# Kernel tuning notes

Hardware: AMD Instinct MI355X
Metric: run time of the kernel (lower is better)

The kernel has to match this reference:

```python
import jax, jax.numpy as jnp
import numpy as np

DIM, H, C = 1024, 16, 64  # dim, num_heads, head_width
B, N = 2, 2048
EPS = 1e-5


def setup_inputs() -> dict:
    key = jax.random.key(0)
    ks = jax.random.split(key, 8)
    x = jax.random.normal(ks[0], (B, N, DIM), dtype=jnp.float32)
    bias = jax.random.normal(ks[1], (B, H, N, N), dtype=jnp.float32)
    mask = jax.random.randint(ks[2], (B, N), 0, 2, dtype=jnp.int32)
    s = DIM ** -0.5
    return {
        'x': x,
        'bias': bias,
        'mask': mask,
        'ln_w': jnp.ones((DIM,), jnp.float32),
        'ln_b': jnp.zeros((DIM,), jnp.float32),
        'w_qkv': jax.random.normal(ks[3], (3 * DIM, DIM), jnp.float32) * s,
        'w_o': jax.random.normal(ks[4], (DIM, DIM), jnp.float32) * s,
        'b_o': jnp.zeros((DIM,), jnp.float32),
        'w_g': jax.random.normal(ks[5], (DIM, DIM), jnp.float32) * s,
        'b_g': jnp.ones((DIM,), jnp.float32),
    }


def reference(x, bias, mask, ln_w, ln_b, w_qkv, w_o, b_o, w_g, b_g):
    # LayerNorm (eps=1e-5)
    mu = jnp.mean(x, axis=-1, keepdims=True)
    var = jnp.mean(jnp.square(x - mu), axis=-1, keepdims=True)
    xn = (x - mu) * jax.lax.rsqrt(var + EPS) * ln_w + ln_b

    # QKV projection (no bias): (B,N,3*DIM) -> (B,H,N,3C), chunk last dim
    t = jnp.einsum('bnd,ed->bne', xn, w_qkv)
    t = t.reshape(B, N, H, 3 * C).transpose(0, 2, 1, 3)  # (B,H,N,3C)
    q, k, v = t[..., :C], t[..., C:2 * C], t[..., 2 * C:]
    q = q * (C ** -0.5)

    # Biased, masked attention scores
    a = jnp.einsum('bhqc,bhkc->bhqk', q, k) + bias
    a = jnp.where(mask[:, None, None, :] == 0, -jnp.inf, a)
    a = jax.nn.softmax(a, axis=-1)

    y = jnp.einsum('bhqk,bhkc->bqhc', a, v).reshape(B, N, DIM)

    # Sigmoid gate from normalized x, then output projection
    g = jax.nn.sigmoid(jnp.einsum('bnd,ed->bne', xn, w_g) + b_g)
    y = g * y
    return jnp.einsum('bnd,ed->bne', y, w_o) + b_o
```

## Files before the change

### kernel.cpp

```cpp
#include <hip/hip_runtime.h>

#define DIMD 1024
#define NHEAD 16
#define CHD 64
#define BBATCH 2
#define NSEQ 2048
#define NTOK 4096
#define KDIM 1024
#define LOG2E 1.4426950408889634f

typedef __attribute__((ext_vector_type(4))) float f32x4;
typedef __attribute__((ext_vector_type(8))) short bf16x8;

__device__ __forceinline__ unsigned short f2bf(float f){
  unsigned int u = __float_as_uint(f);
  u += 0x7fffu + ((u >> 16) & 1u);
  return (unsigned short)(u >> 16);
}
__device__ __forceinline__ float bf2f(unsigned short u){
  return __uint_as_float(((unsigned int)u) << 16);
}

__device__ __forceinline__ void gl2lds16(const void* g, void* l){
  __builtin_amdgcn_global_load_lds(
      (const __attribute__((address_space(1))) unsigned int*)g,
      (__attribute__((address_space(3))) unsigned int*)l, 16, 0, 0);
}

template<int CTRL>
__device__ __forceinline__ float dppmv(float x){
  return __int_as_float(__builtin_amdgcn_mov_dpp(__float_as_int(x), CTRL, 0xF, 0xF, true));
}
__device__ __forceinline__ float rmax16(float x){
  x = fmaxf(x, dppmv<0xB1>(x));
  x = fmaxf(x, dppmv<0x4E>(x));
  x = fmaxf(x, dppmv<0x141>(x));
  x = fmaxf(x, dppmv<0x140>(x));
  return x;
}
__device__ __forceinline__ float rsum16(float x){
  x += dppmv<0xB1>(x);
  x += dppmv<0x4E>(x);
  x += dppmv<0x141>(x);
  x += dppmv<0x140>(x);
  return x;
}

__global__ __launch_bounds__(256) void pre_kernel(const float* __restrict__ x,
    const float* __restrict__ lw, const float* __restrict__ lb,
    const float* __restrict__ wqkv, const float* __restrict__ wg,
    const float* __restrict__ wo, unsigned short* __restrict__ xn,
    unsigned short* __restrict__ Wpack, unsigned short* __restrict__ Wo){
  __shared__ float red[8];
  int t = threadIdx.x;
  if (blockIdx.x < 4096){
    int row = blockIdx.x;
    const float4* xr = (const float4*)(x + (size_t)row * DIMD);
    float4 v = xr[t];
    float s  = v.x + v.y + v.z + v.w;
    float s2 = v.x*v.x + v.y*v.y + v.z*v.z + v.w*v.w;
#pragma unroll
    for (int m = 1; m < 64; m <<= 1){
      s  += __shfl_xor(s,  m, 64);
      s2 += __shfl_xor(s2, m, 64);
    }
    int wv = t >> 6;
    if ((t & 63) == 0){ red[wv] = s; red[wv + 4] = s2; }
    __syncthreads();
    s  = red[0] + red[1] + red[2] + red[3];
    s2 = red[4] + red[5] + red[6] + red[7];
    float mu  = s  * (1.0f / DIMD);
    float var = s2 * (1.0f / DIMD) - mu * mu;
    float rs  = rsqrtf(var + 1e-5f);
    float4 w  = ((const float4*)lw)[t];
    float4 bb = ((const float4*)lb)[t];
    ushort4 o;
    o.x = f2bf((v.x - mu) * rs * w.x + bb.x);
    o.y = f2bf((v.y - mu) * rs * w.y + bb.y);
    o.z = f2bf((v.z - mu) * rs * w.z + bb.z);
    o.w = f2bf((v.w - mu) * rs * w.w + bb.w);
    ((ushort4*)xn)[(size_t)row * 256 + t] = o;
  } else {
    int i = (blockIdx.x - 4096) * 256 + t;
    const int NQP   = 4096 * 1024 / 4;
    const int NQQKV = 3072 * 1024 / 4;
    float4 v; unsigned short* dst;
    if (i < NQP){
      const float* src = (i < NQQKV) ? (wqkv + (size_t)i * 4)
                                     : (wg + (size_t)(i - NQQKV) * 4);
      v = *(const float4*)src;
      dst = Wpack + (size_t)i * 4;
    } else {
      int j = i - NQP;
      v = ((const float4*)wo)[j];
      dst = Wo + (size_t)j * 4;
    }
    ushort4 o = { f2bf(v.x), f2bf(v.y), f2bf(v.z), f2bf(v.w) };
    *(ushort4*)dst = o;
  }
}

__device__ __forceinline__ void gemm_stage(const unsigned short* __restrict__ A,
    const unsigned short* __restrict__ Bm, int m0, int n0, int kb, char* lds, int tid){
#pragma unroll
  for (int i = 0; i < 4; i++){
    int c  = i * 256 + tid;
    int cc = c & 511;
    int r  = cc >> 2, k4 = cc & 3;
    const unsigned short* src =
        ((c >> 9) ? (Bm + (size_t)(n0 + r) * KDIM) : (A + (size_t)(m0 + r) * KDIM))
        + kb + k4 * 8;
    gl2lds16(src, lds + c * 16);
  }
}

__device__ __forceinline__ void gemm_main(const unsigned short* __restrict__ A,
    const unsigned short* __restrict__ Bm, int m0, int n0, char* lds,
    f32x4 acc[4][4], int wm, int wn, int l16, int quad){
  int tid = threadIdx.x;
  gemm_stage(A, Bm, m0, n0, 0, lds, tid);
  for (int kt = 0; kt < 32; kt++){
    __syncthreads();
    if (kt + 1 < 32)
      gemm_stage(A, Bm, m0, n0, (kt + 1) * 32, lds + ((kt + 1) & 1) * 16384, tid);
    const char* Ab = lds + (kt & 1) * 16384;
    const char* Bb = Ab + 8192;
    bf16x8 af[4], bfr[4];
#pragma unroll
    for (int t2 = 0; t2 < 4; t2++){
      af[t2]  = *(const bf16x8*)(Ab + (wm + t2 * 16 + l16) * 64 + quad * 16);
      bfr[t2] = *(const bf16x8*)(Bb + (wn + t2 * 16 + l16) * 64 + quad * 16);
    }
#pragma unroll
    for (int mt = 0; mt < 4; mt++)
#pragma unroll
      for (int nt = 0; nt < 4; nt++)
        acc[mt][nt] = __builtin_amdgcn_mfma_f32_16x16x32_bf16(af[mt], bfr[nt], acc[mt][nt], 0, 0, 0);
  }
}

__global__ __launch_bounds__(256) void gemm_qkvg(const unsigned short* __restrict__ xn,
    const unsigned short* __restrict__ Wpack, const float* __restrict__ bg,
    unsigned short* __restrict__ Q, unsigned short* __restrict__ Ko,
    unsigned short* __restrict__ Vt, unsigned short* __restrict__ g){
  __shared__ char lds[32768];
  int tid = threadIdx.x, lane = tid & 63, wave = tid >> 6;
  int l16 = lane & 15, quad = lane >> 4;
  int wm = (wave & 1) * 64, wn = (wave >> 1) * 64;
  int m0 = blockIdx.y * 128, n0 = blockIdx.x * 128;
  f32x4 acc[4][4];
#pragma unroll
  for (int i = 0; i < 4; i++)
#pragma unroll
    for (int j = 0; j < 4; j++) acc[i][j] = (f32x4){0.f, 0.f, 0.f, 0.f};
  gemm_main(xn, Wpack, m0, n0, lds, acc, wm, wn, l16, quad);
  const float QSCALE = 0.125f * LOG2E;
#pragma unroll
  for (int mt = 0; mt < 4; mt++){
#pragma unroll
    for (int nt = 0; nt < 4; nt++){
      int col = n0 + wn + nt * 16 + l16;
#pragma unroll
      for (int reg = 0; reg < 4; reg++){
        int row = m0 + wm + mt * 16 + quad * 4 + reg;
        float val = acc[mt][nt][reg];
        int b = row >> 11, n = row & 2047;
        if (col < 3072){
          int h = col / 192;
          int r = col - h * 192;
          int bh = b * 16 + h;
          if (r < 64)
            Q[((size_t)bh * 2048 + n) * 64 + r] = f2bf(val * QSCALE);
          else if (r < 128)
            Ko[((size_t)bh * 2048 + n) * 64 + (r - 64)] = f2bf(val);
          else
            Vt[((size_t)bh * 64 + (r - 128)) * 2048 + n] = f2bf(val);
        } else {
          int d = col - 3072;
          float gv = 1.0f / (1.0f + __expf(-(val + bg[d])));
          g[(size_t)row * 1024 + d] = f2bf(gv);
        }
      }
    }
  }
}

__device__ __forceinline__ void attn_stage(const unsigned short* __restrict__ Kbh,
    const unsigned short* __restrict__ Vtbh, int kb, char* Kdst, char* Vdst, int tid){
#pragma unroll
  for (int i = 0; i < 2; i++){
    int l = i * 256 + tid;
    int n = l >> 3, cc = (l & 7) ^ (n & 7);
    gl2lds16(Kbh + (size_t)(kb + n) * 64 + cc * 8, Kdst + l * 16);
  }
#pragma unroll
  for (int i = 0; i < 2; i++){
    int l = i * 256 + tid;
    int c = l >> 3, cc = (l & 7) ^ (c & 7);
    gl2lds16(Vtbh + (size_t)c * 2048 + kb + cc * 8, Vdst + l * 16);
  }
}

__global__ __launch_bounds__(256) void attn_kernel(
    const unsigned short* __restrict__ Q, const unsigned short* __restrict__ Ko,
    const unsigned short* __restrict__ Vt, const float* __restrict__ bias,
    const int* __restrict__ mask, const unsigned short* __restrict__ g,
    unsigned short* __restrict__ yg){
  __shared__ char smem[40960];
  int tid = threadIdx.x, lane = tid & 63, wave = tid >> 6;
  int l16 = lane & 15, quad = lane >> 4;
  int qt = blockIdx.x, bh = blockIdx.y;
  int b = bh >> 4, h = bh & 15;

  const unsigned short* Qbh  = Q  + (size_t)bh * 2048 * 64;
  const unsigned short* Kbh  = Ko + (size_t)bh * 2048 * 64;
  const unsigned short* Vtbh = Vt + (size_t)bh * 64 * 2048;
  const float* biasw = bias + (size_t)bh * 2048 * 2048 + (size_t)(qt * 64 + wave * 16) * 2048;
  const int* maskb = mask + b * 2048;
  char* Pw = smem + 32768 + wave * 2048;

  bf16x8 qf[2];
  {
    const unsigned short* qrow = Qbh + (size_t)(qt * 64 + wave * 16 + l16) * 64;
    qf[0] = *(const bf16x8*)(qrow + quad * 8);
    qf[1] = *(const bf16x8*)(qrow + 32 + quad * 8);
  }

  f32x4 yacc[4];
#pragma unroll
  for (int ct = 0; ct < 4; ct++) yacc[ct] = (f32x4){0.f, 0.f, 0.f, 0.f};
  float m_run[4] = {-1e30f, -1e30f, -1e30f, -1e30f};
  float l_run[4] = {0.f, 0.f, 0.f, 0.f};

  float ba[4][4], bb[4][4];
  int mka[4], mkb[4];
  attn_stage(Kbh, Vtbh, 0, smem, smem + 16384, tid);
#pragma unroll
  for (int nt = 0; nt < 4; nt++){
    mka[nt] = maskb[nt * 16 + l16];
#pragma unroll
    for (int reg = 0; reg < 4; reg++)
      ba[nt][reg] = biasw[(size_t)(quad * 4 + reg) * 2048 + nt * 16 + l16];
  }

  auto body = [&](int kt, float (&cur)[4][4], int (&mcur)[4],
                  float (&nxt)[4][4], int (&mnxt)[4]){
    __syncthreads();
    int kb = kt * 64;
    if (kt + 1 < 32){
      attn_stage(Kbh, Vtbh, kb + 64, smem + (((kt + 1) & 1) << 13),
                 smem + 16384 + (((kt + 1) & 1) << 13), tid);
#pragma unroll
      for (int nt = 0; nt < 4; nt++){
        mnxt[nt] = maskb[kb + 64 + nt * 16 + l16];
#pragma unroll
        for (int reg = 0; reg < 4; reg++)
          nxt[nt][reg] = biasw[(size_t)(quad * 4 + reg) * 2048 + kb + 64 + nt * 16 + l16];
      }
    }
    const char* Kb_ = smem + ((kt & 1) << 13);
    const char* Vb_ = smem + 16384 + ((kt & 1) << 13);

    f32x4 s[4];
#pragma unroll
    for (int nt = 0; nt < 4; nt++) s[nt] = (f32x4){0.f, 0.f, 0.f, 0.f};
#pragma unroll
    for (int kk = 0; kk < 2; kk++)
#pragma unroll
      for (int nt = 0; nt < 4; nt++){
        int n = nt * 16 + l16;
        bf16x8 kf = *(const bf16x8*)(Kb_ + n * 128 + ((((kk << 2) + quad) ^ (n & 7)) << 4));
        s[nt] = __builtin_amdgcn_mfma_f32_16x16x32_bf16(qf[kk], kf, s[nt], 0, 0, 0);
      }
#pragma unroll
    for (int nt = 0; nt < 4; nt++){
      bool ok = (mcur[nt] != 0);
#pragma unroll
      for (int reg = 0; reg < 4; reg++){
        float v = fmaf(cur[nt][reg], LOG2E, s[nt][reg]);
        s[nt][reg] = ok ? v : -1e30f;
      }
    }
    float alpha[4], psum[4];
#pragma unroll
    for (int reg = 0; reg < 4; reg++){
      float m4 = fmaxf(fmaxf(s[0][reg], s[1][reg]), fmaxf(s[2][reg], s[3][reg]));
      m4 = rmax16(m4);
      float mn = fmaxf(m_run[reg], m4);
      alpha[reg] = __builtin_amdgcn_exp2f(m_run[reg] - mn);
      m_run[reg] = mn;
      psum[reg] = 0.f;
    }
#pragma unroll
    for (int nt = 0; nt < 4; nt++){
      int n = nt * 16 + l16;
#pragma unroll
      for (int reg = 0; reg < 4; reg++){
        float p = __builtin_amdgcn_exp2f(s[nt][reg] - m_run[reg]);
        psum[reg] += p;
        int r = quad * 4 + reg;
        unsigned int u = __float_as_uint(p) + 0x8000u;
        *(unsigned short*)(Pw + r * 128 + (((n >> 3) ^ (r & 7)) << 4) + ((n & 7) << 1)) =
            (unsigned short)(u >> 16);
      }
    }
#pragma unroll
    for (int reg = 0; reg < 4; reg++){
      float ps = rsum16(psum[reg]);
      l_run[reg] = l_run[reg] * alpha[reg] + ps;
    }
#pragma unroll
    for (int ct = 0; ct < 4; ct++)
#pragma unroll
      for (int reg = 0; reg < 4; reg++)
        yacc[ct][reg] *= alpha[reg];
    asm volatile("s_waitcnt lgkmcnt(0)" ::: "memory");
#pragma unroll
    for (int kk = 0; kk < 2; kk++){
      bf16x8 pf = *(const bf16x8*)(Pw + l16 * 128 + ((((kk << 2) + quad) ^ (l16 & 7)) << 4));
#pragma unroll
      for (int ct = 0; ct < 4; ct++){
        int c = ct * 16 + l16;
        bf16x8 vf = *(const bf16x8*)(Vb_ + c * 128 + ((((kk << 2) + quad) ^ (c & 7)) << 4));
        yacc[ct] = __builtin_amdgcn_mfma_f32_16x16x32_bf16(pf, vf, yacc[ct], 0, 0, 0);
      }
    }
  };

#pragma unroll 1
  for (int kt2 = 0; kt2 < 16; kt2++){
    body(kt2 * 2,     ba, mka, bb, mkb);
    body(kt2 * 2 + 1, bb, mkb, ba, mka);
  }

  float inv[4];
#pragma unroll
  for (int reg = 0; reg < 4; reg++) inv[reg] = __builtin_amdgcn_rcpf(l_run[reg]);
#pragma unroll
  for (int ct = 0; ct < 4; ct++){
    int d = h * 64 + ct * 16 + l16;
#pragma unroll
    for (int reg = 0; reg < 4; reg++){
      int token = b * 2048 + qt * 64 + wave * 16 + quad * 4 + reg;
      float gv = bf2f(g[(size_t)token * 1024 + d]);
      yg[(size_t)token * 1024 + d] = f2bf(yacc[ct][reg] * inv[reg] * gv);
    }
  }
}

__global__ __launch_bounds__(256) void gemm_out(const unsigned short* __restrict__ yg,
    const unsigned short* __restrict__ Wo, const float* __restrict__ bo,
    float* __restrict__ out){
  __shared__ char lds[32768];
  int tid = threadIdx.x, lane = tid & 63, wave = tid >> 6;
  int l16 = lane & 15, quad = lane >> 4;
  int wm = (wave & 1) * 64, wn = (wave >> 1) * 64;
  int m0 = blockIdx.y * 128, n0 = blockIdx.x * 128;
  f32x4 acc[4][4];
#pragma unroll
  for (int i = 0; i < 4; i++)
#pragma unroll
    for (int j = 0; j < 4; j++) acc[i][j] = (f32x4){0.f, 0.f, 0.f, 0.f};
  gemm_main(yg, Wo, m0, n0, lds, acc, wm, wn, l16, quad);
#pragma unroll
  for (int mt = 0; mt < 4; mt++){
#pragma unroll
    for (int nt = 0; nt < 4; nt++){
      int col = n0 + wn + nt * 16 + l16;
#pragma unroll
      for (int reg = 0; reg < 4; reg++){
        int row = m0 + wm + mt * 16 + quad * 4 + reg;
        out[(size_t)row * 1024 + col] = acc[mt][nt][reg] + bo[col];
      }
    }
  }
}

extern "C" void kernel_launch(void* const* d_in, const int* in_sizes, int n_in,
                              void* d_out, int out_size, void* d_ws, size_t ws_size,
                              hipStream_t stream){
  const float* x    = (const float*)d_in[0];
  const float* bias = (const float*)d_in[1];
  const int*   mask = (const int*)d_in[2];
  const float* lnw  = (const float*)d_in[3];
  const float* lnb  = (const float*)d_in[4];
  const float* wqkv = (const float*)d_in[5];
  const float* wo   = (const float*)d_in[6];
  const float* bo   = (const float*)d_in[7];
  const float* wg   = (const float*)d_in[8];
  const float* bg   = (const float*)d_in[9];
  float* out = (float*)d_out;

  char* ws = (char*)d_ws;
  unsigned short* xn    = (unsigned short*)(ws);
  unsigned short* Wpack = (unsigned short*)(ws + (8u  << 20));
  unsigned short* Wob   = (unsigned short*)(ws + (16u << 20));
  unsigned short* Qb    = (unsigned short*)(ws + (18u << 20));
  unsigned short* Kb    = (unsigned short*)(ws + (26u << 20));
  unsigned short* Vtb   = (unsigned short*)(ws + (34u << 20));
  unsigned short* gb    = (unsigned short*)(ws + (42u << 20));
  unsigned short* ygb   = (unsigned short*)(ws + (50u << 20));

  pre_kernel<<<dim3(9216), dim3(256), 0, stream>>>(x, lnw, lnb, wqkv, wg, wo, xn, Wpack, Wob);
  gemm_qkvg<<<dim3(32, 32), dim3(256), 0, stream>>>(xn, Wpack, bg, Qb, Kb, Vtb, gb);
  attn_kernel<<<dim3(32, 32), dim3(256), 0, stream>>>(Qb, Kb, Vtb, bias, mask, gb, ygb);
  gemm_out<<<dim3(8, 32), dim3(256), 0, stream>>>(ygb, Wob, bo, out);
}
```

Before: 855.3 us.

## Reorder QKV weight rows by class, vectorize epilogue stores, split-K output GEMM

Packs the QKV weight rows so each 128-column GEMM tile maps to a single class (Q, K, V or gate). Each tile's epilogue then takes one uniform branch and can write V transposed with ushort4 stores. The gate sigmoid now uses exp2/rcp intrinsics. The output GEMM goes from 256 blocks to a 2-way split-K (512 blocks) to fill more CUs, with a separate reduction kernel that adds the bias. In exchange it writes and reads 32MB of fp32 partials and adds one extra launch.

```diff
diff --git a/kernel.cpp b/kernel.cpp
--- a/kernel.cpp
+++ b/kernel.cpp
@@ -85,11 +85,16 @@
     const int NQP   = 4096 * 1024 / 4;
     const int NQQKV = 3072 * 1024 / 4;
     float4 v; unsigned short* dst;
-    if (i < NQP){
-      const float* src = (i < NQQKV) ? (wqkv + (size_t)i * 4)
-                                     : (wg + (size_t)(i - NQQKV) * 4);
-      v = *(const float4*)src;
-      dst = Wpack + (size_t)i * 4;
+    if (i < NQQKV){
+      v = ((const float4*)wqkv)[i];
+      int e = i >> 8, k4 = i & 255;
+      int h = e / 192, r = e - h * 192;
+      int e2 = ((r >> 6) << 10) + (h << 6) + (r & 63);
+      dst = Wpack + (size_t)e2 * 1024 + k4 * 4;
+    } else if (i < NQP){
+      int j = i - NQQKV;
+      v = ((const float4*)wg)[j];
+      dst = Wpack + (size_t)3072 * 1024 + (size_t)j * 4;
     } else {
       int j = i - NQP;
       v = ((const float4*)wo)[j];
@@ -115,14 +120,14 @@
 }
 
 __device__ __forceinline__ void gemm_main(const unsigned short* __restrict__ A,
-    const unsigned short* __restrict__ Bm, int m0, int n0, char* lds,
+    const unsigned short* __restrict__ Bm, int m0, int n0, int kt0, int ktn, char* lds,
     f32x4 acc[4][4], int wm, int wn, int l16, int quad){
   int tid = threadIdx.x;
-  gemm_stage(A, Bm, m0, n0, 0, lds, tid);
-  for (int kt = 0; kt < 32; kt++){
+  gemm_stage(A, Bm, m0, n0, kt0 * 32, lds, tid);
+  for (int kt = 0; kt < ktn; kt++){
     __syncthreads();
-    if (kt + 1 < 32)
-      gemm_stage(A, Bm, m0, n0, (kt + 1) * 32, lds + ((kt + 1) & 1) * 16384, tid);
+    if (kt + 1 < ktn)
+      gemm_stage(A, Bm, m0, n0, (kt0 + kt + 1) * 32, lds + ((kt + 1) & 1) * 16384, tid);
     const char* Ab = lds + (kt & 1) * 16384;
     const char* Bb = Ab + 8192;
     bf16x8 af[4], bfr[4];
@@ -153,33 +158,54 @@
   for (int i = 0; i < 4; i++)
 #pragma unroll
     for (int j = 0; j < 4; j++) acc[i][j] = (f32x4){0.f, 0.f, 0.f, 0.f};
-  gemm_main(xn, Wpack, m0, n0, lds, acc, wm, wn, l16, quad);
+  gemm_main(xn, Wpack, m0, n0, 0, 32, lds, acc, wm, wn, l16, quad);
   const float QSCALE = 0.125f * LOG2E;
-#pragma unroll
-  for (int mt = 0; mt < 4; mt++){
-#pragma unroll
-    for (int nt = 0; nt < 4; nt++){
-      int col = n0 + wn + nt * 16 + l16;
-#pragma unroll
-      for (int reg = 0; reg < 4; reg++){
-        int row = m0 + wm + mt * 16 + quad * 4 + reg;
-        float val = acc[mt][nt][reg];
-        int b = row >> 11, n = row & 2047;
-        if (col < 3072){
-          int h = col / 192;
-          int r = col - h * 192;
-          int bh = b * 16 + h;
-          if (r < 64)
-            Q[((size_t)bh * 2048 + n) * 64 + r] = f2bf(val * QSCALE);
-          else if (r < 128)
-            Ko[((size_t)bh * 2048 + n) * 64 + (r - 64)] = f2bf(val);
-          else
-            Vt[((size_t)bh * 64 + (r - 128)) * 2048 + n] = f2bf(val);
-        } else {
-          int d = col - 3072;
-          float gv = 1.0f / (1.0f + __expf(-(val + bg[d])));
-          g[(size_t)row * 1024 + d] = f2bf(gv);
+  int cls = n0 >> 10;
+  if (cls == 2){
+#pragma unroll
+    for (int mt = 0; mt < 4; mt++){
+      int row0 = m0 + wm + mt * 16 + quad * 4;
+      int b = row0 >> 11, n = row0 & 2047;
+#pragma unroll
+      for (int nt = 0; nt < 4; nt++){
+        int cc = (n0 + wn + nt * 16 + l16) & 1023;
+        int h = cc >> 6, c = cc & 63;
+        ushort4 o = { f2bf(acc[mt][nt][0]), f2bf(acc[mt][nt][1]),
+                      f2bf(acc[mt][nt][2]), f2bf(acc[mt][nt][3]) };
+        *(ushort4*)(Vt + ((size_t)((b * 16 + h) * 64 + c) * 2048 + n)) = o;
+      }
+    }
+  } else if (cls == 3){
+#pragma unroll
+    for (int mt = 0; mt < 4; mt++){
+#pragma unroll
+      for (int nt = 0; nt < 4; nt++){
+        int d = (n0 + wn + nt * 16 + l16) & 1023;
+        float bgd = bg[d];
+#pragma unroll
+        for (int reg = 0; reg < 4; reg++){
+          int token = m0 + wm + mt * 16 + quad * 4 + reg;
+          float t2 = -(acc[mt][nt][reg] + bgd) * LOG2E;
+          float gv = __builtin_amdgcn_rcpf(1.0f + __builtin_amdgcn_exp2f(t2));
+          g[(size_t)token * 1024 + d] = f2bf(gv);
         }
+      }
+    }
+  } else {
+    unsigned short* dst = (cls == 0) ? Q : Ko;
+    float sc = (cls == 0) ? QSCALE : 1.0f;
+#pragma unroll
+    for (int mt = 0; mt < 4; mt++){
+      int row0 = m0 + wm + mt * 16 + quad * 4;
+      int b = row0 >> 11, n = row0 & 2047;
+#pragma unroll
+      for (int nt = 0; nt < 4; nt++){
+        int cc = (n0 + wn + nt * 16 + l16) & 1023;
+        int h = cc >> 6, c = cc & 63;
+        size_t base = ((size_t)(b * 16 + h) * 2048 + n) * 64 + c;
+#pragma unroll
+        for (int reg = 0; reg < 4; reg++)
+          dst[base + (size_t)reg * 64] = f2bf(acc[mt][nt][reg] * sc);
       }
     }
   }
@@ -348,20 +374,21 @@
   }
 }
 
-__global__ __launch_bounds__(256) void gemm_out(const unsigned short* __restrict__ yg,
-    const unsigned short* __restrict__ Wo, const float* __restrict__ bo,
-    float* __restrict__ out){
+__global__ __launch_bounds__(256) void gemm_out_sk(const unsigned short* __restrict__ yg,
+    const unsigned short* __restrict__ Wo, float* __restrict__ part){
   __shared__ char lds[32768];
   int tid = threadIdx.x, lane = tid & 63, wave = tid >> 6;
   int l16 = lane & 15, quad = lane >> 4;
   int wm = (wave & 1) * 64, wn = (wave >> 1) * 64;
   int m0 = blockIdx.y * 128, n0 = blockIdx.x * 128;
+  int z = blockIdx.z;
   f32x4 acc[4][4];
 #pragma unroll
   for (int i = 0; i < 4; i++)
 #pragma unroll
     for (int j = 0; j < 4; j++) acc[i][j] = (f32x4){0.f, 0.f, 0.f, 0.f};
-  gemm_main(yg, Wo, m0, n0, lds, acc, wm, wn, l16, quad);
+  gemm_main(yg, Wo, m0, n0, z * 16, 16, lds, acc, wm, wn, l16, quad);
+  float* pz = part + ((size_t)z << 22);
 #pragma unroll
   for (int mt = 0; mt < 4; mt++){
 #pragma unroll
@@ -370,10 +397,20 @@
 #pragma unroll
       for (int reg = 0; reg < 4; reg++){
         int row = m0 + wm + mt * 16 + quad * 4 + reg;
-        out[(size_t)row * 1024 + col] = acc[mt][nt][reg] + bo[col];
-      }
-    }
-  }
+        pz[(size_t)row * 1024 + col] = acc[mt][nt][reg];
+      }
+    }
+  }
+}
+
+__global__ __launch_bounds__(256) void add_out(const float* __restrict__ part,
+    const float* __restrict__ bo, float* __restrict__ out){
+  int i = blockIdx.x * 256 + threadIdx.x;
+  float4 a = ((const float4*)part)[i];
+  float4 b = ((const float4*)(part + (1u << 22)))[i];
+  float4 c = ((const float4*)bo)[i & 255];
+  float4 o = { a.x + b.x + c.x, a.y + b.y + c.y, a.z + b.z + c.z, a.w + b.w + c.w };
+  ((float4*)out)[i] = o;
 }
 
 extern "C" void kernel_launch(void* const* d_in, const int* in_sizes, int n_in,
@@ -400,9 +437,11 @@
   unsigned short* Vtb   = (unsigned short*)(ws + (34u << 20));
   unsigned short* gb    = (unsigned short*)(ws + (42u << 20));
   unsigned short* ygb   = (unsigned short*)(ws + (50u << 20));
+  float*          partb = (float*)(ws + (64u << 20));
 
   pre_kernel<<<dim3(9216), dim3(256), 0, stream>>>(x, lnw, lnb, wqkv, wg, wo, xn, Wpack, Wob);
   gemm_qkvg<<<dim3(32, 32), dim3(256), 0, stream>>>(xn, Wpack, bg, Qb, Kb, Vtb, gb);
   attn_kernel<<<dim3(32, 32), dim3(256), 0, stream>>>(Qb, Kb, Vtb, bias, mask, gb, ygb);
-  gemm_out<<<dim3(8, 32), dim3(256), 0, stream>>>(ygb, Wob, bo, out);
-}
+  gemm_out_sk<<<dim3(8, 32, 2), dim3(256), 0, stream>>>(ygb, Wob, partb);
+  add_out<<<dim3(4096), dim3(256), 0, stream>>>(partb, bo, out);
+}
```

Result: faster. 837.5 us (-2.1%).
